# Performance work log

Hardware: AMD Instinct MI355X
Metric: run time of the kernel (lower is better)

Reference implementation:

```python
import jax, jax.numpy as jnp
import numpy as np

N_HITS = 500_000
LATENT = 256
HITS_PER_TRACK = 10
NUM_TRACKS = N_HITS // HITS_PER_TRACK


def setup_inputs() -> dict:
    key = jax.random.key(0)
    k_h, k_w1, k_w2 = jax.random.split(key, 3)
    scale = 1.0 / np.sqrt(LATENT)
    h = jax.random.normal(k_h, (N_HITS, LATENT), dtype=jnp.float32)
    W1 = jax.random.normal(k_w1, (LATENT, LATENT), dtype=jnp.float32) * scale
    b1 = jnp.zeros((LATENT,), dtype=jnp.float32)
    w2 = jax.random.normal(k_w2, (LATENT,), dtype=jnp.float32) * scale
    b2 = jnp.zeros((), dtype=jnp.float32)
    # 10 hits per track, sorted, no empty segments
    batch_indices = (jnp.arange(N_HITS, dtype=jnp.int32) // HITS_PER_TRACK)
    return {"h": h, "W1": W1, "b1": b1, "w2": w2, "b2": b2,
            "batch_indices": batch_indices, "num_tracks": NUM_TRACKS}


def reference(h, W1, b1, w2, b2, batch_indices, num_tracks):
    # score_net: Linear -> Tanh -> Linear(->1), squeezed
    scores = jnp.tanh(h @ W1 + b1) @ w2 + b2            # (N,)
    # per-segment numerically-stable softmax
    seg_max = jax.ops.segment_max(scores, batch_indices, num_segments=num_tracks)
    e = jnp.exp(scores - seg_max[batch_indices])        # (N,)
    denom = jax.ops.segment_sum(e, batch_indices, num_segments=num_tracks)
    w = e / denom[batch_indices]                         # (N,)
    # per-segment weighted sum of h
    pooled = jax.ops.segment_sum(w[:, None] * h, batch_indices, num_segments=num_tracks)
    return pooled                                        # (num_tracks, LATENT)
```

## Files before the change

### kernel.cpp

```cpp
#include <hip/hip_runtime.h>


typedef __attribute__((ext_vector_type(8))) short short8;
typedef __attribute__((ext_vector_type(4))) float f32x4;

#define LATENT       256
#define HPT          10
#define TPB_TRACKS   16
#define ROWS_PB      (TPB_TRACKS * HPT)
#define STRIPS_PB    (ROWS_PB / 16)
#define WAVES        8
#define THREADS      (WAVES * 64)
#define LOG2E        1.44269504088896f


__device__ __forceinline__ short bf16_rne(float x) {
    unsigned u = __float_as_uint(x);
    u += 0x7FFFu + ((u >> 16) & 1u);
    return (short)(u >> 16);
}

__device__ __forceinline__ float tanh_fast(float x) {
    float e = __builtin_amdgcn_exp2f(x * (2.0f * LOG2E));
    return 1.0f - 2.0f * __builtin_amdgcn_rcpf(e + 1.0f);
}

__global__ __launch_bounds__(256)
void convert_w1_kernel(const float* __restrict__ W1, short* __restrict__ w1t) {
    int idx = blockIdx.x * 256 + threadIdx.x;
    int n = idx & 255;
    int k = (idx >> 8) << 1;
    short2 p;
    p.x = bf16_rne(W1[(size_t)k * LATENT + n]);
    p.y = bf16_rne(W1[(size_t)(k + 1) * LATENT + n]);
    *(short2*)&w1t[n * LATENT + k] = p;
}

__device__ __forceinline__ f32x4 strip_scores(const char* smem, int s, int c, int q,
                                              const short8* bA, const short8* bB,
                                              float b1A, float w2A, float b1B, float w2B)
{
    const int row = s * 16 + c;
    const char* abase = smem + row * 512;
    const int swz = (row & 7) << 4;
    f32x4 acc0 = {0.f, 0.f, 0.f, 0.f};
    f32x4 acc1 = {0.f, 0.f, 0.f, 0.f};
    #pragma unroll
    for (int kt = 0; kt < 8; ++kt) {
        short8 af = *(const short8*)(abase + ((q * 16 + kt * 64) ^ swz));
        acc0 = __builtin_amdgcn_mfma_f32_16x16x32_bf16(af, bA[kt], acc0, 0, 0, 0);
        acc1 = __builtin_amdgcn_mfma_f32_16x16x32_bf16(af, bB[kt], acc1, 0, 0, 0);
    }
    f32x4 part;
    #pragma unroll
    for (int r = 0; r < 4; ++r)
        part[r] = w2A * tanh_fast(acc0[r] + b1A) + w2B * tanh_fast(acc1[r] + b1B);
    #pragma unroll
    for (int r = 0; r < 4; ++r) {
        float v = part[r];
        v += __shfl_xor(v, 1);
        v += __shfl_xor(v, 2);
        v += __shfl_xor(v, 4);
        v += __shfl_xor(v, 8);
        part[r] = v;
    }
    return part;
}

__global__ __launch_bounds__(THREADS, 4)
void softmax_pool_kernel(const float* __restrict__ h,
                         const short* __restrict__ w1t,
                         const float* __restrict__ b1,
                         const float* __restrict__ w2,
                         float* __restrict__ out,
                         int n_hits, int num_tracks)
{
    __shared__ __align__(16) char smem[81920];

    const int tid  = threadIdx.x;
    const int wave = tid >> 6;
    const int lane = tid & 63;
    const int q    = lane >> 4;
    const int c    = lane & 15;
    const int blk  = blockIdx.x;

    {
        const int rsub = tid >> 5;
        const int c8   = tid & 31;
        const float* src0 = h + (size_t)(blk * ROWS_PB + rsub) * LATENT + c8 * 8;
        #pragma unroll 2
        for (int s = 0; s < STRIPS_PB; ++s) {
            const int row = s * 16 + rsub;
            const float* src = src0 + (size_t)s * 16 * LATENT;
            float4 f0 = *(const float4*)src;
            float4 f1 = *(const float4*)(src + 4);
            short8 v;
            v[0] = bf16_rne(f0.x); v[1] = bf16_rne(f0.y);
            v[2] = bf16_rne(f0.z); v[3] = bf16_rne(f0.w);
            v[4] = bf16_rne(f1.x); v[5] = bf16_rne(f1.y);
            v[6] = bf16_rne(f1.z); v[7] = bf16_rne(f1.w);
            int off = (row * 512 + c8 * 16) ^ ((row & 7) << 4);
            *(short8*)(smem + off) = v;
        }
    }

    const int nA = (wave << 5) + c;
    const int nB = nA + 16;
    short8 bA[8], bB[8];
    #pragma unroll
    for (int kt = 0; kt < 8; ++kt) {
        bA[kt] = *(const short8*)(w1t + (size_t)nA * LATENT + q * 8 + kt * 32);
        bB[kt] = *(const short8*)(w1t + (size_t)nB * LATENT + q * 8 + kt * 32);
    }
    #pragma unroll
    for (int kt = 0; kt < 8; ++kt) {
        asm volatile("" : "+v"(bA[kt]));
        asm volatile("" : "+v"(bB[kt]));
    }
    const float b1A = b1[nA], w2A = w2[nA];
    const float b1B = b1[nB], w2B = w2[nB];

    __syncthreads();

    f32x4 p0 = strip_scores(smem, 0, c, q, bA, bB, b1A, w2A, b1B, w2B);
    __syncthreads();
    if (c == 0)
        *(f32x4*)(smem + wave * 640 + q * 16) = p0;

    #pragma unroll 1
    for (int s = 1; s < STRIPS_PB; ++s) {
        f32x4 p = strip_scores(smem, s, c, q, bA, bB, b1A, w2A, b1B, w2B);
        if (c == 0)
            *(f32x4*)(smem + wave * 640 + (s * 16 + q * 4) * 4) = p;
    }
    __syncthreads();

    if (tid < ROWS_PB) {
        float v = 0.f;
        #pragma unroll
        for (int w = 0; w < WAVES; ++w)
            v += *(const float*)(smem + w * 640 + tid * 4);
        *(float*)(smem + 5120 + tid * 4) = v;
    }
    __syncthreads();

    if (tid < TPB_TRACKS) {
        float* scp = (float*)(smem + 5120) + tid * HPT;
        float sv[HPT];
        float m = -1e30f;
        #pragma unroll
        for (int i = 0; i < HPT; ++i) {
            sv[i] = scp[i];
            m = fmaxf(m, sv[i]);
        }
        float sum = 0.f;
        #pragma unroll
        for (int i = 0; i < HPT; ++i) {
            sv[i] = __builtin_amdgcn_exp2f((sv[i] - m) * LOG2E);
            sum += sv[i];
        }
        float inv = __builtin_amdgcn_rcpf(sum);
        #pragma unroll
        for (int i = 0; i < HPT; ++i)
            scp[i] = sv[i] * inv;
    }
    __syncthreads();

    const float* wts = (const float*)(smem + 5120);
    #pragma unroll
    for (int i = 0; i < 2; ++i) {
        int t = wave * 2 + i;
        int tg = blk * TPB_TRACKS + t;
        if (tg >= num_tracks) continue;
        const float* hb = h + (size_t)tg * HPT * LATENT + lane * 4;
        float4 acc = {0.f, 0.f, 0.f, 0.f};
        #pragma unroll
        for (int j = 0; j < HPT; ++j) {
            float wi = wts[t * HPT + j];
            float4 v = *(const float4*)(hb + (size_t)j * LATENT);
            acc.x += wi * v.x;
            acc.y += wi * v.y;
            acc.z += wi * v.z;
            acc.w += wi * v.w;
        }
        *(float4*)(out + (size_t)tg * LATENT + lane * 4) = acc;
    }
}

extern "C" void kernel_launch(void* const* d_in, const int* in_sizes, int n_in,
                              void* d_out, int out_size, void* d_ws, size_t ws_size,
                              hipStream_t stream) {
    const float* h  = (const float*)d_in[0];
    const float* W1 = (const float*)d_in[1];
    const float* b1 = (const float*)d_in[2];
    const float* w2 = (const float*)d_in[3];
    float* out = (float*)d_out;
    short* w1t = (short*)d_ws;

    int n_hits     = in_sizes[0] / LATENT;
    int num_tracks = out_size / LATENT;
    int blocks     = (num_tracks + TPB_TRACKS - 1) / TPB_TRACKS;

    convert_w1_kernel<<<128, 256, 0, stream>>>(W1, w1t);
    softmax_pool_kernel<<<blocks, THREADS, 0, stream>>>(h, w1t, b1, w2, out,
                                                        n_hits, num_tracks);
}
```

Measured before the change: 737.2 us.

## Software-pipeline h strip loads with MFMA score computation

Only the first four strips of h are loaded up front, held in registers, converted to bf16 and staged in LDS. Each later strip's global load is issued before the MFMA score computation of an already staged strip, then converted and written to LDS afterwards. Partial-score writes are delayed by one iteration so they never clobber rows still being read. The aim is to hide global-memory latency behind compute, at the cost of a block barrier per pipelined strip and more live registers.

Result: faster. 722.3 us (-2.0%).

```diff
diff --git a/kernel.cpp b/kernel.cpp
--- a/kernel.cpp
+++ b/kernel.cpp
@@ -11,6 +11,8 @@
 #define STRIPS_PB    (ROWS_PB / 16)
 #define WAVES        8
 #define THREADS      (WAVES * 64)
+#define PRO_STRIPS   4
+#define PIPE_CHUNKS  (STRIPS_PB - PRO_STRIPS)
 #define LOG2E        1.44269504088896f
 
 
@@ -18,6 +20,15 @@
     unsigned u = __float_as_uint(x);
     u += 0x7FFFu + ((u >> 16) & 1u);
     return (short)(u >> 16);
+}
+
+__device__ __forceinline__ short8 pack_bf16x8(float4 f0, float4 f1) {
+    short8 v;
+    v[0] = bf16_rne(f0.x); v[1] = bf16_rne(f0.y);
+    v[2] = bf16_rne(f0.z); v[3] = bf16_rne(f0.w);
+    v[4] = bf16_rne(f1.x); v[5] = bf16_rne(f1.y);
+    v[6] = bf16_rne(f1.z); v[7] = bf16_rne(f1.w);
+    return v;
 }
 
 __device__ __forceinline__ float tanh_fast(float x) {
@@ -84,23 +95,17 @@
     const int c    = lane & 15;
     const int blk  = blockIdx.x;
 
+    const int rsub = tid >> 5;
+    const int c8   = tid & 31;
+
+    float4 pf[2 * PRO_STRIPS];
     {
-        const int rsub = tid >> 5;
-        const int c8   = tid & 31;
-        const float* src0 = h + (size_t)(blk * ROWS_PB + rsub) * LATENT + c8 * 8;
-        #pragma unroll 2
-        for (int s = 0; s < STRIPS_PB; ++s) {
-            const int row = s * 16 + rsub;
+        const float* src0 = h + ((size_t)blk * ROWS_PB + rsub) * LATENT + c8 * 8;
+        #pragma unroll
+        for (int s = 0; s < PRO_STRIPS; ++s) {
             const float* src = src0 + (size_t)s * 16 * LATENT;
-            float4 f0 = *(const float4*)src;
-            float4 f1 = *(const float4*)(src + 4);
-            short8 v;
-            v[0] = bf16_rne(f0.x); v[1] = bf16_rne(f0.y);
-            v[2] = bf16_rne(f0.z); v[3] = bf16_rne(f0.w);
-            v[4] = bf16_rne(f1.x); v[5] = bf16_rne(f1.y);
-            v[6] = bf16_rne(f1.z); v[7] = bf16_rne(f1.w);
-            int off = (row * 512 + c8 * 16) ^ ((row & 7) << 4);
-            *(short8*)(smem + off) = v;
+            pf[2 * s]     = *(const float4*)src;
+            pf[2 * s + 1] = *(const float4*)(src + 4);
         }
     }
 
@@ -120,19 +125,46 @@
     const float b1A = b1[nA], w2A = w2[nA];
     const float b1B = b1[nB], w2B = w2[nB];
 
-    __syncthreads();
-
-    f32x4 p0 = strip_scores(smem, 0, c, q, bA, bB, b1A, w2A, b1B, w2B);
-    __syncthreads();
-    if (c == 0)
-        *(f32x4*)(smem + wave * 640 + q * 16) = p0;
-
+    #pragma unroll
+    for (int s = 0; s < PRO_STRIPS; ++s) {
+        const int row = s * 16 + rsub;
+        short8 v = pack_bf16x8(pf[2 * s], pf[2 * s + 1]);
+        int off = (row * 512 + c8 * 16) ^ ((row & 7) << 4);
+        *(short8*)(smem + off) = v;
+    }
+    __syncthreads();
+
+    f32x4 pprev;
     #pragma unroll 1
-    for (int s = 1; s < STRIPS_PB; ++s) {
+    for (int cch = 0; cch < PIPE_CHUNKS; ++cch) {
+        const int srow = (PRO_STRIPS + cch) * 16 + rsub;
+        const float* src = h + ((size_t)blk * ROWS_PB + srow) * LATENT + c8 * 8;
+        float4 g0 = *(const float4*)src;
+        float4 g1 = *(const float4*)(src + 4);
+        __builtin_amdgcn_sched_barrier(0);
+
+        f32x4 p = strip_scores(smem, cch, c, q, bA, bB, b1A, w2A, b1B, w2B);
+
+        if (cch > 0 && c == 0)
+            *(f32x4*)(smem + wave * 640 + ((cch - 1) * 16 + q * 4) * 4) = pprev;
+        pprev = p;
+
+        short8 v = pack_bf16x8(g0, g1);
+        int off = (srow * 512 + c8 * 16) ^ ((srow & 7) << 4);
+        *(short8*)(smem + off) = v;
+
+        __syncthreads();
+    }
+
+    #pragma unroll 1
+    for (int s = PIPE_CHUNKS; s < STRIPS_PB; ++s) {
         f32x4 p = strip_scores(smem, s, c, q, bA, bB, b1A, w2A, b1B, w2B);
         if (c == 0)
-            *(f32x4*)(smem + wave * 640 + (s * 16 + q * 4) * 4) = p;
-    }
+            *(f32x4*)(smem + wave * 640 + ((s - 1) * 16 + q * 4) * 4) = pprev;
+        pprev = p;
+    }
+    if (c == 0)
+        *(f32x4*)(smem + wave * 640 + ((STRIPS_PB - 1) * 16 + q * 4) * 4) = pprev;
     __syncthreads();
 
     if (tid < ROWS_PB) {
```
